# Kernel tuning notes

Hardware: AMD Instinct MI355X
Metric: run time of the kernel (lower is better)

## Reference

```python
import jax, jax.numpy as jnp
import numpy as np

N = 50000      # nodes
E = 800000     # edges (avg degree 16)
IN, HID, OUT = 128, 256, 64
G = 500        # graphs in the batch (100 nodes each)
NEG_SLOPE = 0.01
EPS = 1e-12


def setup_inputs() -> dict:
    key = jax.random.key(0)
    ks = jax.random.split(key, 9)
    x = jax.random.normal(ks[0], (N, IN), jnp.float32)
    edge_index = jax.random.randint(ks[1], (2, E), 0, N, dtype=jnp.int32)
    # sorted segment ids with every graph present (100 nodes per graph)
    batch = jnp.repeat(jnp.arange(G, dtype=jnp.int32), N // G)
    def lin(k, fan_in, fan_out):
        s = 1.0 / np.sqrt(fan_in)
        kw, kb = jax.random.split(k)
        W = jax.random.uniform(kw, (fan_in, fan_out), jnp.float32, -s, s)
        b = jax.random.uniform(kb, (fan_out,), jnp.float32, -s, s)
        return W, b
    W1, b1 = lin(ks[2], IN, HID)
    W2, b2 = lin(ks[3], HID, HID)
    W3, b3 = lin(ks[4], HID, OUT)
    return {"x": x, "edge_index": edge_index, "batch": batch,
            "W1": W1, "b1": b1, "W2": W2, "b2": b2, "W3": W3, "b3": b3}


def _sage_conv(x, edge_index, W, b):
    # SAGEConv(aggr='add', root_weight=False, normalize=True):
    # gather source features, scatter-add to targets, linear, L2 normalize.
    src, dst = edge_index[0], edge_index[1]
    agg = jax.ops.segment_sum(x[src], dst, num_segments=x.shape[0])  # [N, d_in]
    out = agg @ W + b                                                 # [N, d_out]
    nrm = jnp.linalg.norm(out, axis=-1, keepdims=True)
    return out / jnp.maximum(nrm, EPS)


def reference(x, edge_index, batch, W1, b1, W2, b2, W3, b3):
    h = _sage_conv(x, edge_index, W1, b1)
    h = jax.nn.leaky_relu(h, NEG_SLOPE)          # dropout p=0 -> identity
    h = _sage_conv(h, edge_index, W2, b2)
    h = jax.nn.leaky_relu(h, NEG_SLOPE)
    h = _sage_conv(h, edge_index, W3, b3)
    # get_zero_nodes: first node of each graph (batch sorted, all G present)
    mask = jnp.concatenate([jnp.ones((1,), bool), batch[1:] != batch[:-1]])
    first_idx = jnp.nonzero(mask, size=G)[0]
    return h[first_idx]                          # [G, OUT]
```

## Files before the change

### kernel.cpp

```cpp
#include <hip/hip_runtime.h>

#define N_NODES 50000
#define E_EDGES 800000
#define IN_DIM  128
#define HID_DIM 256
#define OUT_DIM 64
#define G_GRAPHS 500
#define CAP 64
#define NBINS 196
#define BINCAP 5120

typedef __attribute__((ext_vector_type(8))) short short8;
typedef __attribute__((ext_vector_type(4))) float float4v;

__device__ __forceinline__ float bf2f(unsigned short u) {
  union { unsigned int i; float f; } c; c.i = ((unsigned int)u) << 16; return c.f;
}
__device__ __forceinline__ unsigned short f2bf(float f) {
  union { float f; unsigned int i; } c; c.f = f;
  unsigned int x = c.i;
  x += 0x7FFFu + ((x >> 16) & 1u);
  return (unsigned short)(x >> 16);
}
__device__ __forceinline__ unsigned int fbits(float f) {
  union { float f; unsigned int i; } c; c.f = f; return c.i;
}
__device__ __forceinline__ float bits2f(unsigned int u) {
  union { unsigned int i; float f; } c; c.i = u; return c.f;
}


__global__ __launch_bounds__(512) void prep_xconv(
    const int* __restrict__ batch, const float* __restrict__ x,
    unsigned char* __restrict__ is_first, unsigned short* __restrict__ xb) {
  const int t = blockIdx.x * 512 + threadIdx.x;
  const int i = t * 4;
  const float4 v = *(const float4*)(x + i);
  ushort4 u;
  u.x = f2bf(v.x); u.y = f2bf(v.y); u.z = f2bf(v.z); u.w = f2bf(v.w);
  *(ushort4*)(xb + i) = u;
  if (t < N_NODES) {
    is_first[t] = (t == 0 || batch[t] != batch[t - 1]) ? 1 : 0;
  }
}


__global__ __launch_bounds__(256) void prep_edges(
    const int* __restrict__ src, const int* __restrict__ dst,
    const float* __restrict__ W1, const float* __restrict__ W2,
    unsigned int* __restrict__ binbuf, int* __restrict__ bin_next,
    unsigned short* __restrict__ W1t, unsigned short* __restrict__ W2t) {
  const int b = blockIdx.x, tid = threadIdx.x;
  if (b < 200) {
    __shared__ int cnt[NBINS];
    __shared__ int gbase[NBINS];
    for (int i = tid; i < NBINS; i += 256) cnt[i] = 0;
    __syncthreads();
    const int base = b * 4096;
    unsigned int pk[16]; int bp[16];
#pragma unroll
    for (int u = 0; u < 16; ++u) {
      const int e = base + u * 256 + tid;
      bp[u] = -1;
      if (e < E_EDGES) {
        const int d = dst[e];
        const int s = src[e];
        const int bin = d >> 8;
        const int pos = atomicAdd(&cnt[bin], 1);
        pk[u] = ((unsigned int)(d & 255) << 16) | (unsigned int)s;
        bp[u] = (bin << 16) | pos;
      }
    }
    __syncthreads();
    for (int i = tid; i < NBINS; i += 256)
      gbase[i] = atomicAdd(&bin_next[i], cnt[i]);
    __syncthreads();
#pragma unroll
    for (int u = 0; u < 16; ++u) {
      if (bp[u] >= 0) {
        const int bin = bp[u] >> 16, pos = bp[u] & 0xFFFF;
        const int idx = gbase[bin] + pos;
        if (idx < BINCAP) binbuf[bin * BINCAP + idx] = pk[u];
      }
    }
  } else {
    const int t = (b - 200) * 256 + tid;
    if (t < 8192) {
      const int n = t >> 5, k0 = (t & 31) * 4;
      ushort4 o;
      o.x = f2bf(W1[(k0 + 0) * 256 + n]);
      o.y = f2bf(W1[(k0 + 1) * 256 + n]);
      o.z = f2bf(W1[(k0 + 2) * 256 + n]);
      o.w = f2bf(W1[(k0 + 3) * 256 + n]);
      *(ushort4*)&W1t[n * 128 + k0] = o;
    } else {
      const int v2 = t - 8192;
      const int n = v2 >> 6, k0 = (v2 & 63) * 4;
      ushort4 o;
      o.x = f2bf(W2[(k0 + 0) * 256 + n]);
      o.y = f2bf(W2[(k0 + 1) * 256 + n]);
      o.z = f2bf(W2[(k0 + 2) * 256 + n]);
      o.w = f2bf(W2[(k0 + 3) * 256 + n]);
      *(ushort4*)&W2t[n * 256 + k0] = o;
    }
  }
}


__global__ __launch_bounds__(512) void prep2(
    const unsigned int* __restrict__ binbuf, const int* __restrict__ bin_next,
    const int* __restrict__ batch, const unsigned char* __restrict__ is_first,
    int* __restrict__ deg, unsigned short* __restrict__ srcs,
    unsigned short* __restrict__ list2, int* __restrict__ l2cnt) {
  __shared__ unsigned short img[256 * CAP];
  __shared__ int cnt[256];
  const int tid = threadIdx.x;
  const int bin = blockIdx.x;
  if (tid < 256) cnt[tid] = 0;
  __syncthreads();
  const int total = min(bin_next[bin], BINCAP);
  const unsigned int* bb = binbuf + bin * BINCAP;
  for (int i = tid; i < total; i += 512) {
    const unsigned int pk = bb[i];
    const int nl = pk >> 16;
    const int pos = atomicAdd(&cnt[nl], 1);
    if (pos < CAP) img[(nl << 6) + pos] = (unsigned short)(pk & 0xFFFFu);
  }
  __syncthreads();
  const int node0 = bin << 8;
  const int nend = min(N_NODES, node0 + 256);
  if (tid < 256 && node0 + tid < nend) {
    const int c = cnt[tid];
    deg[node0 + tid] = c;
    if (is_first[node0 + tid]) {
      const int g = batch[node0 + tid];
      l2cnt[g] = min(c, CAP);
      unsigned int* d = (unsigned int*)(list2 + g * 64);
      const unsigned int* s = (const unsigned int*)(img + (tid << 6));
      for (int q = 0; q < 32; ++q) d[q] = s[q];
    }
  }
  const int nwords = (nend - node0) * 32;
  unsigned int* dstw = (unsigned int*)(srcs + ((size_t)node0 << 6));
  const unsigned int* srcw = (const unsigned int*)img;
  for (int i = tid; i < nwords; i += 512) dstw[i] = srcw[i];
}


template<int K, int MODE>
__global__ __launch_bounds__(512, 8) void fused_layer(
    const unsigned short* __restrict__ H,
    const int* __restrict__ deg, const unsigned short* __restrict__ srcs,
    const unsigned short* __restrict__ Wt,
    const float* __restrict__ bias,
    unsigned short* __restrict__ Hout,
    const unsigned short* __restrict__ list2,
    const int* __restrict__ l2cnt,
    float* __restrict__ agg_part)
{
  constexpr int M = 256;
  constexpr int TN = 16;
  constexpr int VPT = K / 64;
  constexpr int LDK = K + 8;
  __shared__ unsigned short a_hi[TN][LDK];
  __shared__ unsigned short a_lo[TN][LDK];
  __shared__ float ssq_tot[TN];
  __shared__ float vld_s[TN];
  __shared__ int nid_s[TN];
  const int tid = threadIdx.x;
  const int lane = tid & 63;
  const int wv = tid >> 6;
  const int graph = blockIdx.x % G_GRAPHS;
  const int p = blockIdx.x / G_GRAPHS;

  if constexpr (MODE == 1) {
    if (p * 16 >= l2cnt[graph]) return;
  }

  if (tid < TN) {
    if constexpr (MODE == 1) {
      const int slot = p * 16 + tid;
      const bool vld = slot < l2cnt[graph];
      nid_s[tid] = vld ? (int)list2[graph * 64 + slot] : 0;
      vld_s[tid] = vld ? 1.f : 0.f;
    } else {
      nid_s[tid] = blockIdx.x * TN + tid;
      vld_s[tid] = 1.f;
    }
    ssq_tot[tid] = 0.f;
  }
  __syncthreads();

  const unsigned short* hb = H + lane * VPT;
  const int node0 = __builtin_amdgcn_readfirstlane(nid_s[2 * wv]);
  const int node1 = __builtin_amdgcn_readfirstlane(nid_s[2 * wv + 1]);
  int cnt0 = __builtin_amdgcn_readfirstlane(min(deg[node0], CAP));
  int cnt1 = __builtin_amdgcn_readfirstlane(min(deg[node1], CAP));
  if constexpr (MODE == 1) {
    if (vld_s[2 * wv] == 0.f) cnt0 = 0;
    if (vld_s[2 * wv + 1] == 0.f) cnt1 = 0;
  }
  int idx0 = 0, idx1 = 0;
  if (lane < cnt0) idx0 = srcs[(node0 << 6) + lane];
  if (lane < cnt1) idx1 = srcs[(node1 << 6) + lane];

  float acc0[VPT], acc1[VPT];
#pragma unroll
  for (int q = 0; q < VPT; ++q) { acc0[q] = 0.f; acc1[q] = 0.f; }
  int j0 = 0, j1 = 0;

  if constexpr (VPT == 2) {
    while (j0 + 16 <= cnt0 && j1 + 16 <= cnt1) {
      int s0[16], s1[16];
#pragma unroll
      for (int u = 0; u < 16; ++u) {
        s0[u] = __builtin_amdgcn_readlane(idx0, j0 + u);
        s1[u] = __builtin_amdgcn_readlane(idx1, j1 + u);
      }
      ushort2 r0[16], r1[16];
#pragma unroll
      for (int u = 0; u < 16; ++u) r0[u] = *(const ushort2*)(hb + s0[u] * K);
#pragma unroll
      for (int u = 0; u < 16; ++u) r1[u] = *(const ushort2*)(hb + s1[u] * K);
#pragma unroll
      for (int u = 0; u < 16; ++u) {
        acc0[0] += bf2f(r0[u].x); acc0[1] += bf2f(r0[u].y);
        acc1[0] += bf2f(r1[u].x); acc1[1] += bf2f(r1[u].y);
      }
      j0 += 16; j1 += 16;
    }
  }

#pragma unroll
  for (int i = 0; i < 2; ++i) {
    const int nn = 2 * wv + i;
    const int cnt = i ? cnt1 : cnt0;
    const int idx = i ? idx1 : idx0;
    float (&acc)[VPT] = i ? acc1 : acc0;
    int j = i ? j1 : j0;

    for (; j + 16 <= cnt; j += 16) {
      int s[16];
#pragma unroll
      for (int u = 0; u < 16; ++u) s[u] = __builtin_amdgcn_readlane(idx, j + u);
      if constexpr (VPT == 4) {
        ushort4 r[16];
#pragma unroll
        for (int u = 0; u < 16; ++u) r[u] = *(const ushort4*)(hb + s[u] * K);
#pragma unroll
        for (int u = 0; u < 16; ++u) {
          acc[0] += bf2f(r[u].x); acc[1] += bf2f(r[u].y);
          acc[2] += bf2f(r[u].z); acc[3] += bf2f(r[u].w);
        }
      } else {
        ushort2 r[16];
#pragma unroll
        for (int u = 0; u < 16; ++u) r[u] = *(const ushort2*)(hb + s[u] * K);
#pragma unroll
        for (int u = 0; u < 16; ++u) {
          acc[0] += bf2f(r[u].x); acc[1] += bf2f(r[u].y);
        }
      }
    }
    for (; j < cnt; j += 8) {
      int s[8]; float w[8];
#pragma unroll
      for (int u = 0; u < 8; ++u) {
        const int q = j + u;
        const int qm = (q < cnt) ? q : (cnt - 1);
        s[u] = __builtin_amdgcn_readlane(idx, qm);
        w[u] = (q < cnt) ? 1.f : 0.f;
      }
      if constexpr (VPT == 4) {
        ushort4 r[8];
#pragma unroll
        for (int u = 0; u < 8; ++u) r[u] = *(const ushort4*)(hb + s[u] * K);
#pragma unroll
        for (int u = 0; u < 8; ++u) {
          acc[0] = fmaf(w[u], bf2f(r[u].x), acc[0]);
          acc[1] = fmaf(w[u], bf2f(r[u].y), acc[1]);
          acc[2] = fmaf(w[u], bf2f(r[u].z), acc[2]);
          acc[3] = fmaf(w[u], bf2f(r[u].w), acc[3]);
        }
      } else {
        ushort2 r[8];
#pragma unroll
        for (int u = 0; u < 8; ++u) r[u] = *(const ushort2*)(hb + s[u] * K);
#pragma unroll
        for (int u = 0; u < 8; ++u) {
          acc[0] = fmaf(w[u], bf2f(r[u].x), acc[0]);
          acc[1] = fmaf(w[u], bf2f(r[u].y), acc[1]);
        }
      }
    }

    unsigned short h[VPT], l[VPT];
#pragma unroll
    for (int jj = 0; jj < VPT; ++jj) {
      const unsigned int u = fbits(acc[jj]);
      h[jj] = (unsigned short)(u >> 16);
      const float res = acc[jj] - bits2f(u & 0xFFFF0000u);
      l[jj] = (unsigned short)(fbits(res) >> 16);
    }
    if constexpr (VPT == 4) {
      *(ushort4*)&a_hi[nn][lane * 4] = make_ushort4(h[0], h[1], h[2], h[3]);
      *(ushort4*)&a_lo[nn][lane * 4] = make_ushort4(l[0], l[1], l[2], l[3]);
    } else {
      *(ushort2*)&a_hi[nn][lane * 2] = make_ushort2(h[0], h[1]);
      *(ushort2*)&a_lo[nn][lane * 2] = make_ushort2(l[0], l[1]);
    }
  }
  __syncthreads();

  const int g = lane >> 4;
  const int lc = lane & 15;
  float4v dacc0 = (float4v){0.f, 0.f, 0.f, 0.f};
  float4v dacc1 = (float4v){0.f, 0.f, 0.f, 0.f};
  const unsigned short* W0 = Wt + (size_t)(wv * 16 + lc) * K + g * 8;
  const unsigned short* W1r = Wt + (size_t)((wv + 8) * 16 + lc) * K + g * 8;
#pragma unroll
  for (int ks = 0; ks < K / 32; ++ks) {
    const short8 ah = *(const short8*)&a_hi[lc][ks * 32 + g * 8];
    const short8 al = *(const short8*)&a_lo[lc][ks * 32 + g * 8];
    const short8 b0 = *(const short8*)(W0 + ks * 32);
    const short8 b1 = *(const short8*)(W1r + ks * 32);
    dacc0 = __builtin_amdgcn_mfma_f32_16x16x32_bf16(ah, b0, dacc0, 0, 0, 0);
    dacc0 = __builtin_amdgcn_mfma_f32_16x16x32_bf16(al, b0, dacc0, 0, 0, 0);
    dacc1 = __builtin_amdgcn_mfma_f32_16x16x32_bf16(ah, b1, dacc1, 0, 0, 0);
    dacc1 = __builtin_amdgcn_mfma_f32_16x16x32_bf16(al, b1, dacc1, 0, 0, 0);
  }

  const float bn0 = bias[wv * 16 + lc];
  const float bn1 = bias[(wv + 8) * 16 + lc];
  float4v o0 = dacc0 + bn0;
  float4v o1 = dacc1 + bn1;
  float sq[4];
#pragma unroll
  for (int r = 0; r < 4; ++r) sq[r] = o0[r] * o0[r] + o1[r] * o1[r];
#pragma unroll
  for (int off = 1; off < 16; off <<= 1) {
#pragma unroll
    for (int r = 0; r < 4; ++r) sq[r] += __shfl_xor(sq[r], off);
  }
  if (lc == 0) {
#pragma unroll
    for (int r = 0; r < 4; ++r) atomicAdd(&ssq_tot[g * 4 + r], sq[r]);
  }
  __syncthreads();

  if constexpr (MODE == 0) {
#pragma unroll
    for (int r = 0; r < 4; ++r) {
      const float inv = 1.f / fmaxf(sqrtf(ssq_tot[g * 4 + r]), 1e-12f);
      float v0 = o0[r] * inv;
      float v1 = o1[r] * inv;
      v0 = (v0 >= 0.f) ? v0 : 0.01f * v0;
      v1 = (v1 >= 0.f) ? v1 : 0.01f * v1;
      const int nd = nid_s[g * 4 + r];
      Hout[(size_t)nd * M + wv * 16 + lc] = f2bf(v0);
      Hout[(size_t)nd * M + (wv + 8) * 16 + lc] = f2bf(v1);
    }
  } else {
    float s0 = 0.f, s1 = 0.f;
#pragma unroll
    for (int r = 0; r < 4; ++r) {
      const float inv = 1.f / fmaxf(sqrtf(ssq_tot[g * 4 + r]), 1e-12f);
      float v0 = o0[r] * inv;
      float v1 = o1[r] * inv;
      v0 = (v0 >= 0.f) ? v0 : 0.01f * v0;
      v1 = (v1 >= 0.f) ? v1 : 0.01f * v1;
      const float w = vld_s[g * 4 + r];
      s0 += w * v0; s1 += w * v1;
    }
    s0 += __shfl_xor(s0, 16); s0 += __shfl_xor(s0, 32);
    s1 += __shfl_xor(s1, 16); s1 += __shfl_xor(s1, 32);
    if (lane < 16) {
      float* pp = agg_part + ((size_t)(graph * 4 + p) << 8);
      pp[wv * 16 + lane] = s0;
      pp[128 + wv * 16 + lane] = s1;
    }
  }
}


__global__ __launch_bounds__(64) void layer3_kernel(
    const float* __restrict__ agg_part,
    const int* __restrict__ l2cnt,
    const float* __restrict__ W,
    const float* __restrict__ bias,
    float* __restrict__ out)
{
  __shared__ float a_s[HID_DIM];
  const int g = blockIdx.x;
  const int lane = threadIdx.x;
  const int nq = (min(l2cnt[g], CAP) + 15) >> 4;
  const float* pp = agg_part + ((size_t)g << 10);
#pragma unroll
  for (int c = 0; c < 4; ++c) {
    const int idx = c * 64 + lane;
    float s = 0.f;
    for (int q = 0; q < nq; ++q) s += pp[q * 256 + idx];
    a_s[idx] = s;
  }
  __syncthreads();
  float o = bias[lane];
#pragma unroll 8
  for (int k = 0; k < HID_DIM; ++k) o += a_s[k] * W[k * OUT_DIM + lane];
  float ss = o * o;
#pragma unroll
  for (int off = 32; off > 0; off >>= 1) ss += __shfl_xor(ss, off);
  const float inv = 1.f / fmaxf(sqrtf(ss), 1e-12f);
  out[(size_t)g * OUT_DIM + lane] = o * inv;
}


extern "C" void kernel_launch(void* const* d_in, const int* in_sizes, int n_in,
                              void* d_out, int out_size, void* d_ws, size_t ws_size,
                              hipStream_t stream) {
  (void)in_sizes; (void)n_in; (void)out_size; (void)ws_size;
  const float* x   = (const float*)d_in[0];
  const int* ei    = (const int*)d_in[1];
  const int* batch = (const int*)d_in[2];
  const float* W1  = (const float*)d_in[3];
  const float* b1  = (const float*)d_in[4];
  const float* W2  = (const float*)d_in[5];
  const float* b2  = (const float*)d_in[6];
  const float* W3  = (const float*)d_in[7];
  const float* b3  = (const float*)d_in[8];
  const int* src = ei;
  const int* dst = ei + E_EDGES;

  char* ws = (char*)d_ws;
  size_t off = 0;
  auto alloc = [&](size_t bytes) {
    void* p = ws + off;
    off = (off + bytes + 255) & ~(size_t)255;
    return p;
  };
  int* bin_next = (int*)alloc((size_t)NBINS * 4);
  const size_t zero_len = off;

  int* deg    = (int*)alloc((size_t)N_NODES * 4);
  unsigned short* srcs = (unsigned short*)alloc((size_t)N_NODES * CAP * 2);
  unsigned char* is_first = (unsigned char*)alloc((size_t)N_NODES);
  unsigned short* list2 = (unsigned short*)alloc((size_t)G_GRAPHS * CAP * 2);
  int* l2cnt  = (int*)alloc((size_t)G_GRAPHS * 4);
  unsigned int* binbuf = (unsigned int*)alloc((size_t)NBINS * BINCAP * 4);
  float* agg_part = (float*)alloc((size_t)G_GRAPHS * 4 * 256 * 4);
  unsigned short* W1t = (unsigned short*)alloc((size_t)256 * 128 * 2);
  unsigned short* W2t = (unsigned short*)alloc((size_t)256 * 256 * 2);
  unsigned short* xb = (unsigned short*)alloc((size_t)N_NODES * IN_DIM * 2);
  unsigned short* h1 = (unsigned short*)alloc((size_t)N_NODES * HID_DIM * 2);

  hipMemsetAsync(bin_next, 0, zero_len, stream);

  prep_xconv<<<3125, 512, 0, stream>>>(batch, x, is_first, xb);
  prep_edges<<<296, 256, 0, stream>>>(src, dst, W1, W2, binbuf, bin_next, W1t, W2t);
  prep2<<<NBINS, 512, 0, stream>>>(binbuf, bin_next, batch, is_first,
                                   deg, srcs, list2, l2cnt);

  fused_layer<IN_DIM, 0><<<N_NODES / 16, 512, 0, stream>>>(
      xb, deg, srcs, W1t, b1, h1, nullptr, nullptr, nullptr);
  fused_layer<HID_DIM, 1><<<G_GRAPHS * 4, 512, 0, stream>>>(
      h1, deg, srcs, W2t, b2, nullptr, list2, l2cnt, agg_part);
  layer3_kernel<<<G_GRAPHS, 64, 0, stream>>>(agg_part, l2cnt, W3, b3, (float*)d_out);
}
```

Before: 198.4 us.

## Fold prep and layer-3 kernels into neighbours to cut launch count

Moves the x-to-bf16 conversion into extra blocks of prep2 and the is_first computation into extra blocks of prep_edges, removing one prep kernel. Folds the layer-3 linear plus normalize into the layer-2 kernel using a per-graph atomic completion counter, so the last block for each graph does the final reduction. This removes two kernel launches and their inter-kernel gaps. The cost is a threadfence, an atomic and an extra barrier per block, a serial tail in the last block of each graph, and graphs with no layer-2 nodes now always launch one block.

Measured after the change: 340.2 us. 71.5% more time.

```diff
diff --git a/kernel.cpp b/kernel.cpp
--- a/kernel.cpp
+++ b/kernel.cpp
@@ -30,25 +30,12 @@
 }
 
 
-__global__ __launch_bounds__(512) void prep_xconv(
-    const int* __restrict__ batch, const float* __restrict__ x,
-    unsigned char* __restrict__ is_first, unsigned short* __restrict__ xb) {
-  const int t = blockIdx.x * 512 + threadIdx.x;
-  const int i = t * 4;
-  const float4 v = *(const float4*)(x + i);
-  ushort4 u;
-  u.x = f2bf(v.x); u.y = f2bf(v.y); u.z = f2bf(v.z); u.w = f2bf(v.w);
-  *(ushort4*)(xb + i) = u;
-  if (t < N_NODES) {
-    is_first[t] = (t == 0 || batch[t] != batch[t - 1]) ? 1 : 0;
-  }
-}
-
-
 __global__ __launch_bounds__(256) void prep_edges(
     const int* __restrict__ src, const int* __restrict__ dst,
+    const int* __restrict__ batch,
     const float* __restrict__ W1, const float* __restrict__ W2,
     unsigned int* __restrict__ binbuf, int* __restrict__ bin_next,
+    unsigned char* __restrict__ is_first,
     unsigned short* __restrict__ W1t, unsigned short* __restrict__ W2t) {
   const int b = blockIdx.x, tid = threadIdx.x;
   if (b < 200) {
@@ -83,7 +70,7 @@
         if (idx < BINCAP) binbuf[bin * BINCAP + idx] = pk[u];
       }
     }
-  } else {
+  } else if (b < 296) {
     const int t = (b - 200) * 256 + tid;
     if (t < 8192) {
       const int n = t >> 5, k0 = (t & 31) * 4;
@@ -103,6 +90,10 @@
       o.w = f2bf(W2[(k0 + 3) * 256 + n]);
       *(ushort4*)&W2t[n * 256 + k0] = o;
     }
+  } else {
+    const int t = (b - 296) * 256 + tid;
+    if (t < N_NODES)
+      is_first[t] = (t == 0 || batch[t] != batch[t - 1]) ? 1 : 0;
   }
 }
 
@@ -110,12 +101,23 @@
 __global__ __launch_bounds__(512) void prep2(
     const unsigned int* __restrict__ binbuf, const int* __restrict__ bin_next,
     const int* __restrict__ batch, const unsigned char* __restrict__ is_first,
+    const float* __restrict__ x, unsigned short* __restrict__ xb,
     int* __restrict__ deg, unsigned short* __restrict__ srcs,
     unsigned short* __restrict__ list2, int* __restrict__ l2cnt) {
   __shared__ unsigned short img[256 * CAP];
   __shared__ int cnt[256];
   const int tid = threadIdx.x;
-  const int bin = blockIdx.x;
+  const int b = blockIdx.x;
+  if (b >= NBINS) {
+    const int t = (b - NBINS) * 512 + tid;
+    const int i = t * 4;
+    const float4 v = *(const float4*)(x + i);
+    ushort4 u;
+    u.x = f2bf(v.x); u.y = f2bf(v.y); u.z = f2bf(v.z); u.w = f2bf(v.w);
+    *(ushort4*)(xb + i) = u;
+    return;
+  }
+  const int bin = b;
   if (tid < 256) cnt[tid] = 0;
   __syncthreads();
   const int total = min(bin_next[bin], BINCAP);
@@ -156,7 +158,11 @@
     unsigned short* __restrict__ Hout,
     const unsigned short* __restrict__ list2,
     const int* __restrict__ l2cnt,
-    float* __restrict__ agg_part)
+    float* __restrict__ agg_part,
+    int* __restrict__ done,
+    const float* __restrict__ W3,
+    const float* __restrict__ b3,
+    float* __restrict__ out)
 {
   constexpr int M = 256;
   constexpr int TN = 16;
@@ -167,6 +173,7 @@
   __shared__ float ssq_tot[TN];
   __shared__ float vld_s[TN];
   __shared__ int nid_s[TN];
+  __shared__ int lastflag;
   const int tid = threadIdx.x;
   const int lane = tid & 63;
   const int wv = tid >> 6;
@@ -174,7 +181,7 @@
   const int p = blockIdx.x / G_GRAPHS;
 
   if constexpr (MODE == 1) {
-    if (p * 16 >= l2cnt[graph]) return;
+    if (p > 0 && p * 16 >= l2cnt[graph]) return;
   }
 
   if (tid < TN) {
@@ -379,38 +386,39 @@
       pp[wv * 16 + lane] = s0;
       pp[128 + wv * 16 + lane] = s1;
     }
-  }
-}
-
-
-__global__ __launch_bounds__(64) void layer3_kernel(
-    const float* __restrict__ agg_part,
-    const int* __restrict__ l2cnt,
-    const float* __restrict__ W,
-    const float* __restrict__ bias,
-    float* __restrict__ out)
-{
-  __shared__ float a_s[HID_DIM];
-  const int g = blockIdx.x;
-  const int lane = threadIdx.x;
-  const int nq = (min(l2cnt[g], CAP) + 15) >> 4;
-  const float* pp = agg_part + ((size_t)g << 10);
-#pragma unroll
-  for (int c = 0; c < 4; ++c) {
-    const int idx = c * 64 + lane;
-    float s = 0.f;
-    for (int q = 0; q < nq; ++q) s += pp[q * 256 + idx];
-    a_s[idx] = s;
-  }
-  __syncthreads();
-  float o = bias[lane];
+
+    const int nq = max(1, (min(l2cnt[graph], CAP) + 15) >> 4);
+    __threadfence();
+    __syncthreads();
+    if (tid == 0)
+      lastflag = (atomicAdd(&done[graph], 1) == nq - 1) ? 1 : 0;
+    __syncthreads();
+    if (lastflag) {
+      __threadfence();
+      float* a_s = (float*)&a_hi[0][0];
+      if (tid < 64) {
+#pragma unroll
+        for (int c = 0; c < 4; ++c) {
+          const int idx = c * 64 + tid;
+          float s = 0.f;
+          for (int q = 0; q < nq; ++q)
+            s += agg_part[((size_t)(graph * 4 + q) << 8) + idx];
+          a_s[idx] = s;
+        }
+      }
+      __syncthreads();
+      if (tid < 64) {
+        float o = b3[tid];
 #pragma unroll 8
-  for (int k = 0; k < HID_DIM; ++k) o += a_s[k] * W[k * OUT_DIM + lane];
-  float ss = o * o;
-#pragma unroll
-  for (int off = 32; off > 0; off >>= 1) ss += __shfl_xor(ss, off);
-  const float inv = 1.f / fmaxf(sqrtf(ss), 1e-12f);
-  out[(size_t)g * OUT_DIM + lane] = o * inv;
+        for (int k = 0; k < HID_DIM; ++k) o += a_s[k] * W3[k * OUT_DIM + tid];
+        float ss = o * o;
+#pragma unroll
+        for (int off2 = 32; off2 > 0; off2 >>= 1) ss += __shfl_xor(ss, off2);
+        const float inv = 1.f / fmaxf(sqrtf(ss), 1e-12f);
+        out[(size_t)graph * OUT_DIM + tid] = o * inv;
+      }
+    }
+  }
 }
 
 
@@ -438,6 +446,7 @@
     return p;
   };
   int* bin_next = (int*)alloc((size_t)NBINS * 4);
+  int* done     = (int*)alloc((size_t)G_GRAPHS * 4);
   const size_t zero_len = off;
 
   int* deg    = (int*)alloc((size_t)N_NODES * 4);
@@ -454,14 +463,15 @@
 
   hipMemsetAsync(bin_next, 0, zero_len, stream);
 
-  prep_xconv<<<3125, 512, 0, stream>>>(batch, x, is_first, xb);
-  prep_edges<<<296, 256, 0, stream>>>(src, dst, W1, W2, binbuf, bin_next, W1t, W2t);
-  prep2<<<NBINS, 512, 0, stream>>>(binbuf, bin_next, batch, is_first,
-                                   deg, srcs, list2, l2cnt);
+  prep_edges<<<492, 256, 0, stream>>>(src, dst, batch, W1, W2,
+                                      binbuf, bin_next, is_first, W1t, W2t);
+  prep2<<<NBINS + 3125, 512, 0, stream>>>(binbuf, bin_next, batch, is_first,
+                                          x, xb, deg, srcs, list2, l2cnt);
 
   fused_layer<IN_DIM, 0><<<N_NODES / 16, 512, 0, stream>>>(
-      xb, deg, srcs, W1t, b1, h1, nullptr, nullptr, nullptr);
+      xb, deg, srcs, W1t, b1, h1, nullptr, nullptr, nullptr,
+      nullptr, nullptr, nullptr, nullptr);
   fused_layer<HID_DIM, 1><<<G_GRAPHS * 4, 512, 0, stream>>>(
-      h1, deg, srcs, W2t, b2, nullptr, list2, l2cnt, agg_part);
-  layer3_kernel<<<G_GRAPHS, 64, 0, stream>>>(agg_part, l2cnt, W3, b3, (float*)d_out);
-}
+      h1, deg, srcs, W2t, b2, nullptr, list2, l2cnt, agg_part,
+      done, W3, b3, (float*)d_out);
+}
```
